# Kernel optimization log

Measured on AMD Instinct MI355X. Metric: run time of the kernel, lower is better.

## Reference

```python
import jax, jax.numpy as jnp
import numpy as np

B, L, H, N = 4, 4096, 1024, 64
LN_EPS = 1e-5


def setup_inputs() -> dict:
    key = jax.random.key(0)
    ks = jax.random.split(key, 6)
    x = jax.random.normal(ks[0], (B, L, H), dtype=jnp.float32)
    # S4D-Lin style init
    log_A_real = jnp.log(0.5 * jnp.ones((H, N), dtype=jnp.float32))
    A_imag = jnp.broadcast_to(jnp.pi * jnp.arange(N, dtype=jnp.float32), (H, N))
    C_re = jax.random.normal(ks[1], (H, N), dtype=jnp.float32) * 0.5
    C_im = jax.random.normal(ks[2], (H, N), dtype=jnp.float32) * 0.5
    # dt log-uniform in [1e-3, 1e-1]
    u = jax.random.uniform(ks[3], (H,), dtype=jnp.float32)
    log_dt = u * (jnp.log(0.1) - jnp.log(0.001)) + jnp.log(0.001)
    D = jax.random.normal(ks[4], (H,), dtype=jnp.float32)
    ln_w = jnp.ones((H,), dtype=jnp.float32)
    ln_b = jnp.zeros((H,), dtype=jnp.float32)
    return {"x": x, "log_A_real": log_A_real, "A_imag": A_imag,
            "C_re": C_re, "C_im": C_im, "log_dt": log_dt, "D": D,
            "ln_w": ln_w, "ln_b": ln_b}


def _s4d_kernel(log_A_real, A_imag, C_re, C_im, log_dt, length):
    # A: [H, N] complex with negative real part (stability)
    A = -jnp.exp(log_A_real) + 1j * A_imag
    dt = jnp.exp(log_dt)[:, None]                      # [H, 1]
    dtA = dt * A                                       # [H, N]
    C = C_re + 1j * C_im                               # [H, N]
    # ZOH discretization: Bbar*C -> C * (exp(dtA)-1)/A
    Ct = C * (jnp.exp(dtA) - 1.0) / A                  # [H, N]
    l = jnp.arange(length, dtype=jnp.float32)
    # Vandermonde: exp(dtA * l) over [H, N, L]
    V = jnp.exp(dtA[:, :, None] * l[None, None, :])
    K = 2.0 * jnp.real(jnp.einsum('hn,hnl->hl', Ct, V))  # [H, L]
    return K


def reference(x, log_A_real, A_imag, C_re, C_im, log_dt, D, ln_w, ln_b):
    b, length, h = x.shape
    K = _s4d_kernel(log_A_real, A_imag, C_re, C_im, log_dt, length)  # [H, L]
    # causal convolution via FFT, channels last: x is [B, L, H]
    n = 2 * length
    Xf = jnp.fft.rfft(x, n=n, axis=1)                  # [B, n//2+1, H]
    Kf = jnp.fft.rfft(K, n=n, axis=1)                  # [H, n//2+1]
    y = jnp.fft.irfft(Xf * Kf.T[None, :, :], n=n, axis=1)[:, :length, :]
    z = y + x * D[None, None, :]
    # dropout is identity in eval mode; residual + LayerNorm
    r = x + z
    mu = jnp.mean(r, axis=-1, keepdims=True)
    var = jnp.var(r, axis=-1, keepdims=True)
    out = (r - mu) * jax.lax.rsqrt(var + LN_EPS) * ln_w + ln_b
    return out
```

## Files before the change

### kernel.cpp

```cpp
#include <hip/hip_runtime.h>
#include <cstdint>

#define Bb 4
#define Lseq 4096
#define Hh 1024
#define Nst 64
constexpr float LN_EPS = 1e-5f;

typedef _Float16 f16x8 __attribute__((ext_vector_type(8)));
typedef _Float16 f16x4 __attribute__((ext_vector_type(4)));
typedef float f32x4v __attribute__((ext_vector_type(4)));

__global__ __launch_bounds__(256) void k_precompute(
    const float* __restrict__ logA, const float* __restrict__ Aim,
    const float* __restrict__ Cre, const float* __restrict__ Cim,
    const float* __restrict__ logdt, _Float16* __restrict__ mats,
    float* __restrict__ wwR, float* __restrict__ wwI) {
    __shared__ float sdAr[64], sdAi[64], scR[64], scI[64], sK[64];
    const int h = blockIdx.x, tid = threadIdx.x;
    _Float16* g = mats + (size_t)h * 20480;

    if (tid < 64) {
        const int n = tid, idx = h * 64 + n;
        const float ar = -__expf(logA[idx]), ai = Aim[idx];
        const float dt = __expf(logdt[h]);
        const float dAr = dt * ar, dAi = dt * ai;
        float sn, cs;
        __sincosf(dAi, &sn, &cs);
        const float em = __expf(dAr);
        const float wr = em * cs, wi = em * sn;
        const float Er = wr - 1.0f, Ei = wi;
        const float cr = Cre[idx], ci = Cim[idx];
        const float nr = cr * Er - ci * Ei, ni = cr * Ei + ci * Er;
        const float invd = 1.0f / (ar * ar + ai * ai);
        const float CtR = (nr * ar + ni * ai) * invd;
        const float CtI = (ni * ar - nr * ai) * invd;
        sdAr[n] = dAr; sdAi[n] = dAi; scR[n] = 2.0f * CtR; scI[n] = 2.0f * CtI;
        float sn2, cs2;
        __sincosf(dAi * 64.0f, &sn2, &cs2);
        const float e64 = __expf(dAr * 64.0f);
        wwR[idx] = e64 * cs2;
        wwI[idx] = e64 * sn2;
    }
    __syncthreads();

    for (int e = tid; e < 4096; e += 256) {
        const int row = e >> 6, colj = e & 63;
        {
            const float p = (float)(63 - colj);
            float sn, cs;
            __sincosf(sdAi[row] * p, &sn, &cs);
            const float ee = __expf(sdAr[row] * p);
            g[e]        = (_Float16)(ee * cs);
            g[4096 + e] = (_Float16)(ee * sn);
        }
        {
            const int n = colj;
            const float q = (float)(row + 1);
            float sn, cs;
            __sincosf(sdAi[n] * q, &sn, &cs);
            const float ee = __expf(sdAr[n] * q);
            const float wRq = ee * cs, wIq = ee * sn;
            g[12288 + e] = (_Float16)(scR[n] * wRq - scI[n] * wIq);
            g[16384 + e] = (_Float16)(-(scR[n] * wIq + scI[n] * wRq));
        }
    }
    if (tid < 64) {
        const float tau = (float)tid;
        float sum = 0.0f;
        for (int n = 0; n < 64; ++n) {
            float sn, cs;
            __sincosf(sdAi[n] * tau, &sn, &cs);
            const float ee = __expf(sdAr[n] * tau);
            sum += ee * (scR[n] * cs - scI[n] * sn);
        }
        sK[tid] = sum;
    }
    __syncthreads();
    for (int e = tid; e < 4096; e += 256) {
        const int t = e >> 6, j = e & 63;
        g[8192 + e] = (j <= t) ? (_Float16)sK[t - j] : (_Float16)0.0f;
    }
}

__global__ __launch_bounds__(256) void k_transpose(const float* __restrict__ x,
                                                   float* __restrict__ xt) {
    __shared__ float tile[32][33];
    const int h0 = blockIdx.x * 32;
    const int l0 = blockIdx.y * 32;
    const int b  = blockIdx.z;
    const int tj = threadIdx.x & 31;
    const int ti = threadIdx.x >> 5;

    const float* src = x + ((size_t)b * Lseq + l0) * Hh + h0;
#pragma unroll
    for (int it = 0; it < 4; ++it) {
        int row = it * 8 + ti;
        tile[row][tj] = src[(size_t)row * Hh + tj];
    }
    __syncthreads();
    float* dst = xt + ((size_t)b * Hh + h0) * Lseq + l0;
#pragma unroll
    for (int it = 0; it < 4; ++it) {
        int row = it * 8 + ti;
        dst[(size_t)row * Lseq + tj] = tile[tj][row];
    }
}

#define MR0 0
#define MI0 9216
#define MM1 18432
#define MPR 27648
#define MPI 36864
#define uRo 46080
#define uIo 55296

#define LFRAG(base, row0, kk) \
    (*(const f16x8*)(sm + (base) + ((row0) + col) * 144 + ((kk) + qd * 8) * 2))

__global__ __launch_bounds__(256, 2) void k_chunk(
    float* __restrict__ xt, const _Float16* __restrict__ mats,
    const float* __restrict__ wwR, const float* __restrict__ wwI,
    const float* __restrict__ Dp) {
    __shared__ __align__(16) unsigned char sm[64512];
    const int tid = threadIdx.x, lane = tid & 63, wv = tid >> 6;
    const int h = blockIdx.x;
    const _Float16* g = mats + (size_t)h * 20480;
    const int col = lane & 15, qd = lane >> 4;
    const int band = wv * 16;

#pragma unroll
    for (int it = 0; it < 10; ++it) {
        const int chunk = it * 256 + tid;
        const int m = chunk >> 9;
        const int rem = chunk & 511;
        const int r = rem >> 3, c16 = rem & 7;
        *(uint4*)(sm + m * 9216 + r * 144 + c16 * 16) =
            *(const uint4*)(g + (size_t)chunk * 8);
    }

    const float Dp1 = 1.0f + Dp[h];
    float swR = 0.0f, swI = 0.0f;
    if (lane < 16) {
        swR = wwR[h * 64 + wv * 16 + lane];
        swI = wwI[h * 64 + wv * 16 + lane];
    }
    __syncthreads();

    for (int b = 0; b < Bb; ++b) {
        float* xr = xt + ((size_t)b * Hh + h) * Lseq;

        f16x8 axk[2];
        f32x4v aR[4] = {}, aI[4] = {};
#pragma unroll
        for (int kh2 = 0; kh2 < 2; ++kh2) {
            const int kk = kh2 * 32;
            const float* xp = xr + (band + col) * 64 + kk + qd * 8;
            const float4 v0 = *(const float4*)(xp);
            const float4 v1 = *(const float4*)(xp + 4);
            f16x8 a;
            a[0] = (_Float16)v0.x; a[1] = (_Float16)v0.y;
            a[2] = (_Float16)v0.z; a[3] = (_Float16)v0.w;
            a[4] = (_Float16)v1.x; a[5] = (_Float16)v1.y;
            a[6] = (_Float16)v1.z; a[7] = (_Float16)v1.w;
            axk[kh2] = a;
#pragma unroll
            for (int nt = 0; nt < 4; ++nt) {
                aR[nt] = __builtin_amdgcn_mfma_f32_16x16x32_f16(
                    a, LFRAG(MR0, nt * 16, kk), aR[nt], 0, 0, 0);
                aI[nt] = __builtin_amdgcn_mfma_f32_16x16x32_f16(
                    a, LFRAG(MI0, nt * 16, kk), aI[nt], 0, 0, 0);
            }
        }
        __syncthreads();
#pragma unroll
        for (int nt = 0; nt < 4; ++nt)
#pragma unroll
            for (int rg = 0; rg < 4; ++rg) {
                const int c = band + qd * 4 + rg, n = nt * 16 + col;
                *(_Float16*)(sm + uRo + c * 144 + n * 2) = (_Float16)aR[nt][rg];
                *(_Float16*)(sm + uIo + c * 144 + n * 2) = (_Float16)aI[nt][rg];
            }
        __syncthreads();

        if (lane < 16) {
            const int n = wv * 16 + lane;
            float sR = 0.0f, sI = 0.0f;
            for (int c = 0; c < 64; ++c) {
                _Float16* pR = (_Float16*)(sm + uRo + c * 144 + n * 2);
                _Float16* pI = (_Float16*)(sm + uIo + c * 144 + n * 2);
                const float uRv = (float)*pR;
                const float uIv = (float)*pI;
                *pR = (_Float16)sR;
                *pI = (_Float16)sI;
                const float nR = fmaf(swR, sR, fmaf(-swI, sI, uRv));
                sI = fmaf(swR, sI, fmaf(swI, sR, uIv));
                sR = nR;
            }
        }
        __syncthreads();

        f32x4v acc[4] = {};
#pragma unroll
        for (int kh2 = 0; kh2 < 2; ++kh2) {
            const int kk = kh2 * 32;
#pragma unroll
            for (int tt = 0; tt < 4; ++tt)
                acc[tt] = __builtin_amdgcn_mfma_f32_16x16x32_f16(
                    axk[kh2], LFRAG(MM1, tt * 16, kk), acc[tt], 0, 0, 0);
        }
#pragma unroll
        for (int kh2 = 0; kh2 < 2; ++kh2) {
            const int kk = kh2 * 32;
            const f16x8 as = LFRAG(uRo, band, kk);
#pragma unroll
            for (int tt = 0; tt < 4; ++tt)
                acc[tt] = __builtin_amdgcn_mfma_f32_16x16x32_f16(
                    as, LFRAG(MPR, tt * 16, kk), acc[tt], 0, 0, 0);
        }
#pragma unroll
        for (int kh2 = 0; kh2 < 2; ++kh2) {
            const int kk = kh2 * 32;
            const f16x8 az = LFRAG(uIo, band, kk);
#pragma unroll
            for (int tt = 0; tt < 4; ++tt)
                acc[tt] = __builtin_amdgcn_mfma_f32_16x16x32_f16(
                    az, LFRAG(MPI, tt * 16, kk), acc[tt], 0, 0, 0);
        }

#pragma unroll
        for (int tt = 0; tt < 4; ++tt)
#pragma unroll
            for (int rg = 0; rg < 4; ++rg) {
                const int l = (band + qd * 4 + rg) * 64 + tt * 16 + col;
                xr[l] = fmaf(xr[l], Dp1, acc[tt][rg]);
            }
    }
}

__global__ __launch_bounds__(512, 2) void k_ln(const float* __restrict__ rt,
                                               float* __restrict__ out,
                                               const float* __restrict__ lnw,
                                               const float* __restrict__ lnb) {
    __shared__ float tile[16 * 1032];
    __shared__ float ps[32][17], pq[32][17];
    __shared__ float mm[16], rs[16];
    const int b  = blockIdx.y;
    const int l0 = blockIdx.x * 16;
    const int tid = threadIdx.x;
    const int ll = tid & 15;
    const int hh = tid >> 4;

    const float* base = rt + (size_t)b * Hh * Lseq + l0;

    float psum = 0.0f, psq = 0.0f;
#pragma unroll 8
    for (int hc = 0; hc < Hh; hc += 32) {
        const float v = base[(size_t)(hc + hh) * Lseq + ll];
        tile[ll * 1032 + hc + hh] = v;
        psum += v;
        psq = fmaf(v, v, psq);
    }
    ps[hh][ll] = psum;
    pq[hh][ll] = psq;
    __syncthreads();
    if (tid < 16) {
        float s = 0.f, q = 0.f;
#pragma unroll
        for (int k = 0; k < 32; ++k) {
            s += ps[k][tid];
            q += pq[k][tid];
        }
        const float mu  = s * (1.0f / Hh);
        const float var = fmaf(-mu, mu, q * (1.0f / Hh));
        mm[tid] = mu;
        rs[tid] = rsqrtf(var + LN_EPS);
    }
    __syncthreads();

    const float w0 = lnw[tid],       b0 = lnb[tid];
    const float w1 = lnw[512 + tid], b1 = lnb[512 + tid];
    float* obase = out + ((size_t)b * Lseq + l0) * Hh;
#pragma unroll 4
    for (int l = 0; l < 16; ++l) {
        const float mu = mm[l], rsg = rs[l];
        const float v0 = tile[l * 1032 + tid];
        const float v1 = tile[l * 1032 + 512 + tid];
        obase[(size_t)l * Hh + tid]       = fmaf((v0 - mu) * rsg, w0, b0);
        obase[(size_t)l * Hh + 512 + tid] = fmaf((v1 - mu) * rsg, w1, b1);
    }
}

extern "C" void kernel_launch(void* const* d_in, const int* in_sizes, int n_in,
                              void* d_out, int out_size, void* d_ws, size_t ws_size,
                              hipStream_t stream) {
    const float* x     = (const float*)d_in[0];
    const float* logA  = (const float*)d_in[1];
    const float* Aim   = (const float*)d_in[2];
    const float* Cre   = (const float*)d_in[3];
    const float* Cim   = (const float*)d_in[4];
    const float* logdt = (const float*)d_in[5];
    const float* Dp    = (const float*)d_in[6];
    const float* lnw   = (const float*)d_in[7];
    const float* lnb   = (const float*)d_in[8];
    float* out = (float*)d_out;
    float* ws  = (float*)d_ws;

    _Float16* mats = (_Float16*)d_out;
    float* wwR = (float*)((char*)d_out + 41943040);
    float* wwI = (float*)((char*)d_out + 42205184);

    k_precompute<<<dim3(Hh), 256, 0, stream>>>(logA, Aim, Cre, Cim, logdt,
                                               mats, wwR, wwI);
    k_transpose<<<dim3(Hh / 32, Lseq / 32, Bb), 256, 0, stream>>>(x, ws);
    k_chunk<<<dim3(Hh), 256, 0, stream>>>(ws, mats, wwR, wwI, Dp);
    k_ln<<<dim3(Lseq / 16, Bb), 512, 0, stream>>>(ws, out, lnw, lnb);
}
```

Measured before the change: 235.9 us.

## Parallelize batches across wave groups in chunk kernel and widen transpose tiles

The chunk kernel goes from 256 to 1024 threads per block, and each group of four waves handles one batch element at the same time instead of looping over the four batches in sequence. Each group gets its own slice of shared memory for the chunk state, which raises LDS use to about 117 KB per block. The transpose kernel moves to 64x64 tiles with float4 global loads and stores, and the LayerNorm tile row stride changes from 1032 to 1033 to reduce bank conflicts. The precompute kernel replaces sincos with separate __sinf/__cosf calls; the large LDS footprint and the 1024-thread bound may limit occupancy.

```diff
diff --git a/kernel.cpp b/kernel.cpp
--- a/kernel.cpp
+++ b/kernel.cpp
@@ -25,10 +25,8 @@
         const float ar = -__expf(logA[idx]), ai = Aim[idx];
         const float dt = __expf(logdt[h]);
         const float dAr = dt * ar, dAi = dt * ai;
-        float sn, cs;
-        __sincosf(dAi, &sn, &cs);
         const float em = __expf(dAr);
-        const float wr = em * cs, wi = em * sn;
+        const float wr = em * __cosf(dAi), wi = em * __sinf(dAi);
         const float Er = wr - 1.0f, Ei = wi;
         const float cr = Cre[idx], ci = Cim[idx];
         const float nr = cr * Er - ci * Ei, ni = cr * Ei + ci * Er;
@@ -36,11 +34,9 @@
         const float CtR = (nr * ar + ni * ai) * invd;
         const float CtI = (ni * ar - nr * ai) * invd;
         sdAr[n] = dAr; sdAi[n] = dAi; scR[n] = 2.0f * CtR; scI[n] = 2.0f * CtI;
-        float sn2, cs2;
-        __sincosf(dAi * 64.0f, &sn2, &cs2);
-        const float e64 = __expf(dAr * 64.0f);
-        wwR[idx] = e64 * cs2;
-        wwI[idx] = e64 * sn2;
+        const float e64 = __expf(dAr * 64.0f), a64 = dAi * 64.0f;
+        wwR[idx] = e64 * __cosf(a64);
+        wwI[idx] = e64 * __sinf(a64);
     }
     __syncthreads();
 
@@ -48,19 +44,15 @@
         const int row = e >> 6, colj = e & 63;
         {
             const float p = (float)(63 - colj);
-            float sn, cs;
-            __sincosf(sdAi[row] * p, &sn, &cs);
-            const float ee = __expf(sdAr[row] * p);
-            g[e]        = (_Float16)(ee * cs);
-            g[4096 + e] = (_Float16)(ee * sn);
+            const float ee = __expf(sdAr[row] * p), ang = sdAi[row] * p;
+            g[e]        = (_Float16)(ee * __cosf(ang));
+            g[4096 + e] = (_Float16)(ee * __sinf(ang));
         }
         {
             const int n = colj;
             const float q = (float)(row + 1);
-            float sn, cs;
-            __sincosf(sdAi[n] * q, &sn, &cs);
-            const float ee = __expf(sdAr[n] * q);
-            const float wRq = ee * cs, wIq = ee * sn;
+            const float ee = __expf(sdAr[n] * q), ang = sdAi[n] * q;
+            const float wRq = ee * __cosf(ang), wIq = ee * __sinf(ang);
             g[12288 + e] = (_Float16)(scR[n] * wRq - scI[n] * wIq);
             g[16384 + e] = (_Float16)(-(scR[n] * wIq + scI[n] * wRq));
         }
@@ -69,10 +61,8 @@
         const float tau = (float)tid;
         float sum = 0.0f;
         for (int n = 0; n < 64; ++n) {
-            float sn, cs;
-            __sincosf(sdAi[n] * tau, &sn, &cs);
-            const float ee = __expf(sdAr[n] * tau);
-            sum += ee * (scR[n] * cs - scI[n] * sn);
+            const float ee = __expf(sdAr[n] * tau), ang = sdAi[n] * tau;
+            sum += ee * (scR[n] * __cosf(ang) - scI[n] * __sinf(ang));
         }
         sK[tid] = sum;
     }
@@ -85,25 +75,28 @@
 
 __global__ __launch_bounds__(256) void k_transpose(const float* __restrict__ x,
                                                    float* __restrict__ xt) {
-    __shared__ float tile[32][33];
-    const int h0 = blockIdx.x * 32;
-    const int l0 = blockIdx.y * 32;
-    const int b  = blockIdx.z;
-    const int tj = threadIdx.x & 31;
-    const int ti = threadIdx.x >> 5;
-
-    const float* src = x + ((size_t)b * Lseq + l0) * Hh + h0;
+    __shared__ float tile[64 * 65];
+    const int h0 = blockIdx.x * 64, l0 = blockIdx.y * 64, b = blockIdx.z;
+    const int c = threadIdx.x & 15, r = threadIdx.x >> 4;
+
+    const float* src = x + ((size_t)(b * Lseq + l0 + r)) * Hh + h0 + 4 * c;
 #pragma unroll
     for (int it = 0; it < 4; ++it) {
-        int row = it * 8 + ti;
-        tile[row][tj] = src[(size_t)row * Hh + tj];
-    }
-    __syncthreads();
-    float* dst = xt + ((size_t)b * Hh + h0) * Lseq + l0;
+        const float4 v = *(const float4*)(src + (size_t)it * 16 * Hh);
+        const int l = it * 16 + r;
+        tile[(4 * c + 0) * 65 + l] = v.x;
+        tile[(4 * c + 1) * 65 + l] = v.y;
+        tile[(4 * c + 2) * 65 + l] = v.z;
+        tile[(4 * c + 3) * 65 + l] = v.w;
+    }
+    __syncthreads();
+    float* dst = xt + ((size_t)(b * Hh + h0 + r)) * Lseq + l0 + 4 * c;
 #pragma unroll
     for (int it = 0; it < 4; ++it) {
-        int row = it * 8 + ti;
-        dst[(size_t)row * Lseq + tj] = tile[tj][row];
+        const float* trow = tile + (it * 16 + r) * 65 + 4 * c;
+        float4 o;
+        o.x = trow[0]; o.y = trow[1]; o.z = trow[2]; o.w = trow[3];
+        *(float4*)(dst + (size_t)it * 16 * Lseq) = o;
     }
 }
 
@@ -112,137 +105,138 @@
 #define MM1 18432
 #define MPR 27648
 #define MPI 36864
-#define uRo 46080
-#define uIo 55296
+#define USB 46080
 
 #define LFRAG(base, row0, kk) \
     (*(const f16x8*)(sm + (base) + ((row0) + col) * 144 + ((kk) + qd * 8) * 2))
 
-__global__ __launch_bounds__(256, 2) void k_chunk(
+__global__ __launch_bounds__(1024, 4) void k_chunk(
     float* __restrict__ xt, const _Float16* __restrict__ mats,
     const float* __restrict__ wwR, const float* __restrict__ wwI,
     const float* __restrict__ Dp) {
-    __shared__ __align__(16) unsigned char sm[64512];
+    __shared__ __align__(16) unsigned char sm[119808];
     const int tid = threadIdx.x, lane = tid & 63, wv = tid >> 6;
+    const int grp = wv >> 2;
+    const int wb  = wv & 3;
     const int h = blockIdx.x;
     const _Float16* g = mats + (size_t)h * 20480;
     const int col = lane & 15, qd = lane >> 4;
-    const int band = wv * 16;
-
-#pragma unroll
-    for (int it = 0; it < 10; ++it) {
-        const int chunk = it * 256 + tid;
-        const int m = chunk >> 9;
-        const int rem = chunk & 511;
-        const int r = rem >> 3, c16 = rem & 7;
-        *(uint4*)(sm + m * 9216 + r * 144 + c16 * 16) =
-            *(const uint4*)(g + (size_t)chunk * 8);
+    const int band = wb * 16;
+    const int uRo = USB + grp * 18432;
+    const int uIo = uRo + 9216;
+
+#pragma unroll
+    for (int it = 0; it < 3; ++it) {
+        const int chunk = it * 1024 + tid;
+        if (chunk < 2560) {
+            const int m = chunk >> 9;
+            const int rem = chunk & 511;
+            const int r = rem >> 3, c16 = rem & 7;
+            *(uint4*)(sm + m * 9216 + r * 144 + c16 * 16) =
+                *(const uint4*)(g + (size_t)chunk * 8);
+        }
     }
 
     const float Dp1 = 1.0f + Dp[h];
     float swR = 0.0f, swI = 0.0f;
     if (lane < 16) {
-        swR = wwR[h * 64 + wv * 16 + lane];
-        swI = wwI[h * 64 + wv * 16 + lane];
-    }
-    __syncthreads();
-
-    for (int b = 0; b < Bb; ++b) {
-        float* xr = xt + ((size_t)b * Hh + h) * Lseq;
-
-        f16x8 axk[2];
-        f32x4v aR[4] = {}, aI[4] = {};
-#pragma unroll
-        for (int kh2 = 0; kh2 < 2; ++kh2) {
-            const int kk = kh2 * 32;
-            const float* xp = xr + (band + col) * 64 + kk + qd * 8;
-            const float4 v0 = *(const float4*)(xp);
-            const float4 v1 = *(const float4*)(xp + 4);
-            f16x8 a;
-            a[0] = (_Float16)v0.x; a[1] = (_Float16)v0.y;
-            a[2] = (_Float16)v0.z; a[3] = (_Float16)v0.w;
-            a[4] = (_Float16)v1.x; a[5] = (_Float16)v1.y;
-            a[6] = (_Float16)v1.z; a[7] = (_Float16)v1.w;
-            axk[kh2] = a;
-#pragma unroll
-            for (int nt = 0; nt < 4; ++nt) {
-                aR[nt] = __builtin_amdgcn_mfma_f32_16x16x32_f16(
-                    a, LFRAG(MR0, nt * 16, kk), aR[nt], 0, 0, 0);
-                aI[nt] = __builtin_amdgcn_mfma_f32_16x16x32_f16(
-                    a, LFRAG(MI0, nt * 16, kk), aI[nt], 0, 0, 0);
-            }
-        }
-        __syncthreads();
-#pragma unroll
-        for (int nt = 0; nt < 4; ++nt)
-#pragma unroll
-            for (int rg = 0; rg < 4; ++rg) {
-                const int c = band + qd * 4 + rg, n = nt * 16 + col;
-                *(_Float16*)(sm + uRo + c * 144 + n * 2) = (_Float16)aR[nt][rg];
-                *(_Float16*)(sm + uIo + c * 144 + n * 2) = (_Float16)aI[nt][rg];
-            }
-        __syncthreads();
-
-        if (lane < 16) {
-            const int n = wv * 16 + lane;
-            float sR = 0.0f, sI = 0.0f;
-            for (int c = 0; c < 64; ++c) {
-                _Float16* pR = (_Float16*)(sm + uRo + c * 144 + n * 2);
-                _Float16* pI = (_Float16*)(sm + uIo + c * 144 + n * 2);
-                const float uRv = (float)*pR;
-                const float uIv = (float)*pI;
-                *pR = (_Float16)sR;
-                *pI = (_Float16)sI;
-                const float nR = fmaf(swR, sR, fmaf(-swI, sI, uRv));
-                sI = fmaf(swR, sI, fmaf(swI, sR, uIv));
-                sR = nR;
-            }
-        }
-        __syncthreads();
-
-        f32x4v acc[4] = {};
-#pragma unroll
-        for (int kh2 = 0; kh2 < 2; ++kh2) {
-            const int kk = kh2 * 32;
-#pragma unroll
-            for (int tt = 0; tt < 4; ++tt)
-                acc[tt] = __builtin_amdgcn_mfma_f32_16x16x32_f16(
-                    axk[kh2], LFRAG(MM1, tt * 16, kk), acc[tt], 0, 0, 0);
-        }
-#pragma unroll
-        for (int kh2 = 0; kh2 < 2; ++kh2) {
-            const int kk = kh2 * 32;
-            const f16x8 as = LFRAG(uRo, band, kk);
-#pragma unroll
-            for (int tt = 0; tt < 4; ++tt)
-                acc[tt] = __builtin_amdgcn_mfma_f32_16x16x32_f16(
-                    as, LFRAG(MPR, tt * 16, kk), acc[tt], 0, 0, 0);
-        }
-#pragma unroll
-        for (int kh2 = 0; kh2 < 2; ++kh2) {
-            const int kk = kh2 * 32;
-            const f16x8 az = LFRAG(uIo, band, kk);
-#pragma unroll
-            for (int tt = 0; tt < 4; ++tt)
-                acc[tt] = __builtin_amdgcn_mfma_f32_16x16x32_f16(
-                    az, LFRAG(MPI, tt * 16, kk), acc[tt], 0, 0, 0);
-        }
-
+        swR = wwR[h * 64 + band + lane];
+        swI = wwI[h * 64 + band + lane];
+    }
+    float* xr = xt + ((size_t)grp * Hh + h) * Lseq;
+    __syncthreads();
+
+    f16x8 axk[2];
+    f32x4v aR[4] = {}, aI[4] = {};
+#pragma unroll
+    for (int kh2 = 0; kh2 < 2; ++kh2) {
+        const int kk = kh2 * 32;
+        const float* xp = xr + (band + col) * 64 + kk + qd * 8;
+        const float4 v0 = *(const float4*)(xp);
+        const float4 v1 = *(const float4*)(xp + 4);
+        f16x8 a;
+        a[0] = (_Float16)v0.x; a[1] = (_Float16)v0.y;
+        a[2] = (_Float16)v0.z; a[3] = (_Float16)v0.w;
+        a[4] = (_Float16)v1.x; a[5] = (_Float16)v1.y;
+        a[6] = (_Float16)v1.z; a[7] = (_Float16)v1.w;
+        axk[kh2] = a;
+#pragma unroll
+        for (int nt = 0; nt < 4; ++nt) {
+            aR[nt] = __builtin_amdgcn_mfma_f32_16x16x32_f16(
+                a, LFRAG(MR0, nt * 16, kk), aR[nt], 0, 0, 0);
+            aI[nt] = __builtin_amdgcn_mfma_f32_16x16x32_f16(
+                a, LFRAG(MI0, nt * 16, kk), aI[nt], 0, 0, 0);
+        }
+    }
+#pragma unroll
+    for (int nt = 0; nt < 4; ++nt)
+#pragma unroll
+        for (int rg = 0; rg < 4; ++rg) {
+            const int cc = band + qd * 4 + rg, n = nt * 16 + col;
+            *(_Float16*)(sm + uRo + cc * 144 + n * 2) = (_Float16)aR[nt][rg];
+            *(_Float16*)(sm + uIo + cc * 144 + n * 2) = (_Float16)aI[nt][rg];
+        }
+    __syncthreads();
+
+    if (lane < 16) {
+        const int n = band + lane;
+        float sR = 0.0f, sI = 0.0f;
+        for (int c = 0; c < 64; ++c) {
+            _Float16* pR = (_Float16*)(sm + uRo + c * 144 + n * 2);
+            _Float16* pI = (_Float16*)(sm + uIo + c * 144 + n * 2);
+            const float uRv = (float)*pR;
+            const float uIv = (float)*pI;
+            *pR = (_Float16)sR;
+            *pI = (_Float16)sI;
+            const float nR = fmaf(swR, sR, fmaf(-swI, sI, uRv));
+            sI = fmaf(swR, sI, fmaf(swI, sR, uIv));
+            sR = nR;
+        }
+    }
+    __syncthreads();
+
+    f32x4v acc[4] = {};
+#pragma unroll
+    for (int kh2 = 0; kh2 < 2; ++kh2) {
+        const int kk = kh2 * 32;
 #pragma unroll
         for (int tt = 0; tt < 4; ++tt)
-#pragma unroll
-            for (int rg = 0; rg < 4; ++rg) {
-                const int l = (band + qd * 4 + rg) * 64 + tt * 16 + col;
-                xr[l] = fmaf(xr[l], Dp1, acc[tt][rg]);
-            }
-    }
+            acc[tt] = __builtin_amdgcn_mfma_f32_16x16x32_f16(
+                axk[kh2], LFRAG(MM1, tt * 16, kk), acc[tt], 0, 0, 0);
+    }
+#pragma unroll
+    for (int kh2 = 0; kh2 < 2; ++kh2) {
+        const int kk = kh2 * 32;
+        const f16x8 as = LFRAG(uRo, band, kk);
+#pragma unroll
+        for (int tt = 0; tt < 4; ++tt)
+            acc[tt] = __builtin_amdgcn_mfma_f32_16x16x32_f16(
+                as, LFRAG(MPR, tt * 16, kk), acc[tt], 0, 0, 0);
+    }
+#pragma unroll
+    for (int kh2 = 0; kh2 < 2; ++kh2) {
+        const int kk = kh2 * 32;
+        const f16x8 az = LFRAG(uIo, band, kk);
+#pragma unroll
+        for (int tt = 0; tt < 4; ++tt)
+            acc[tt] = __builtin_amdgcn_mfma_f32_16x16x32_f16(
+                az, LFRAG(MPI, tt * 16, kk), acc[tt], 0, 0, 0);
+    }
+
+#pragma unroll
+    for (int tt = 0; tt < 4; ++tt)
+#pragma unroll
+        for (int rg = 0; rg < 4; ++rg) {
+            const int l = (band + qd * 4 + rg) * 64 + tt * 16 + col;
+            xr[l] = fmaf(xr[l], Dp1, acc[tt][rg]);
+        }
 }
 
 __global__ __launch_bounds__(512, 2) void k_ln(const float* __restrict__ rt,
                                                float* __restrict__ out,
                                                const float* __restrict__ lnw,
                                                const float* __restrict__ lnb) {
-    __shared__ float tile[16 * 1032];
+    __shared__ float tile[16 * 1033];
     __shared__ float ps[32][17], pq[32][17];
     __shared__ float mm[16], rs[16];
     const int b  = blockIdx.y;
@@ -257,7 +251,7 @@
 #pragma unroll 8
     for (int hc = 0; hc < Hh; hc += 32) {
         const float v = base[(size_t)(hc + hh) * Lseq + ll];
-        tile[ll * 1032 + hc + hh] = v;
+        tile[ll * 1033 + hc + hh] = v;
         psum += v;
         psq = fmaf(v, v, psq);
     }
@@ -284,8 +278,8 @@
 #pragma unroll 4
     for (int l = 0; l < 16; ++l) {
         const float mu = mm[l], rsg = rs[l];
-        const float v0 = tile[l * 1032 + tid];
-        const float v1 = tile[l * 1032 + 512 + tid];
+        const float v0 = tile[l * 1033 + tid];
+        const float v1 = tile[l * 1033 + 512 + tid];
         obase[(size_t)l * Hh + tid]       = fmaf((v0 - mu) * rsg, w0, b0);
         obase[(size_t)l * Hh + 512 + tid] = fmaf((v1 - mu) * rsg, w1, b1);
     }
@@ -312,7 +306,7 @@
 
     k_precompute<<<dim3(Hh), 256, 0, stream>>>(logA, Aim, Cre, Cim, logdt,
                                                mats, wwR, wwI);
-    k_transpose<<<dim3(Hh / 32, Lseq / 32, Bb), 256, 0, stream>>>(x, ws);
-    k_chunk<<<dim3(Hh), 256, 0, stream>>>(ws, mats, wwR, wwI, Dp);
+    k_transpose<<<dim3(Hh / 64, Lseq / 64, Bb), 256, 0, stream>>>(x, ws);
+    k_chunk<<<dim3(Hh), 1024, 0, stream>>>(ws, mats, wwR, wwI, Dp);
     k_ln<<<dim3(Lseq / 16, Bb), 512, 0, stream>>>(ws, out, lnw, lnb);
 }
```

Result: no change. 233.4 us (-1.1%).
